# Kernel optimization log

Measured on AMD Instinct MI355X. Metric: run time of the kernel, lower is better.

## Reference

```python
import jax, jax.numpy as jnp
import numpy as np

N_NODES = 15000
N_EDGES = 400000
H_DIM = 128
N_RELS = 237
N_BASES = 100


def rel_graph_conv(x, src, dst, etype, norm, V, comp, loop_w, bias, n_nodes):
    """DGL RelGraphConv with basis regularizer, self_loop=True, bias=True.

    W_r = sum_b comp[r, b] * V[b]; message m_e = (x[src_e] @ W_{etype_e}) * norm_e;
    h[v] = sum_{e: dst_e = v} m_e + x[v] @ loop_w + bias.
    Reordered as sum over bases to avoid materializing per-edge weights:
      h = sum_b segment_sum(coef[etype, b] * norm * x[src], dst) @ V[b]
    """
    x_src = x[src] * norm                      # [E, D] (norm is [E, 1])
    coef = comp[etype]                         # [E, B]
    d_out = V.shape[2]

    def body(acc, cv):
        c, Vb = cv                             # c: [E], Vb: [D, Dout]
        agg = jax.ops.segment_sum(x_src * c[:, None], dst, num_segments=n_nodes)
        return acc + agg @ Vb, None

    init = jnp.zeros((n_nodes, d_out), x.dtype)
    h, _ = jax.lax.scan(body, init, (coef.T, V))  # scan over B bases
    return h + bias + x @ loop_w


def setup_inputs() -> dict:
    key = jax.random.key(0)
    ks = jax.random.split(key, 16)
    s = 1.0 / np.sqrt(H_DIM)
    inp = {
        "nids": jnp.arange(N_NODES, dtype=jnp.int32),
        "src": jax.random.randint(ks[0], (N_EDGES,), 0, N_NODES),
        "dst": jax.random.randint(ks[1], (N_EDGES,), 0, N_NODES),
        "etype": jax.random.randint(ks[2], (N_EDGES,), 0, N_RELS),
        "norm": jax.random.uniform(ks[3], (N_EDGES, 1), dtype=jnp.float32),
        "edge_weights": jax.random.normal(ks[4], (N_EDGES,), dtype=jnp.float32),
        "emb": jax.random.normal(ks[5], (N_NODES, H_DIM), dtype=jnp.float32) * s,
        "V1": jax.random.normal(ks[6], (N_BASES, H_DIM, H_DIM), dtype=jnp.float32) * s,
        "comp1": jax.random.normal(ks[7], (N_RELS, N_BASES), dtype=jnp.float32) * (1.0 / np.sqrt(N_BASES)),
        "loop1": jax.random.normal(ks[8], (H_DIM, H_DIM), dtype=jnp.float32) * s,
        "bias1": jnp.zeros((H_DIM,), dtype=jnp.float32),
        "V2": jax.random.normal(ks[9], (N_BASES, H_DIM, H_DIM), dtype=jnp.float32) * s,
        "comp2": jax.random.normal(ks[10], (N_RELS, N_BASES), dtype=jnp.float32) * (1.0 / np.sqrt(N_BASES)),
        "loop2": jax.random.normal(ks[11], (H_DIM, H_DIM), dtype=jnp.float32) * s,
        "bias2": jnp.zeros((H_DIM,), dtype=jnp.float32),
    }
    return inp


def reference(nids, src, dst, etype, norm, edge_weights, emb, V1, comp1, loop1, bias1, V2, comp2, loop2, bias2):
    # edge_weights is accepted but unused by the original forward.
    x = emb[nids]                                              # embedding lookup
    n = x.shape[0]
    h = jax.nn.relu(rel_graph_conv(x, src, dst, etype, norm, V1, comp1, loop1, bias1, n))
    # dropout(p=0.2) treated as identity (eval mode)
    h = rel_graph_conv(h, src, dst, etype, norm, V2, comp2, loop2, bias2, n)
    return h
```

## Files before the change

kernel.cpp:

```cpp
#include <hip/hip_runtime.h>
#include <hip/hip_bf16.h>


typedef unsigned short u16;
typedef unsigned int   u32;
typedef __bf16 bf16x8 __attribute__((ext_vector_type(8)));
typedef float  f32x4  __attribute__((ext_vector_type(4)));
typedef u32    u32x2  __attribute__((ext_vector_type(2)));

#define N_NODES 15000
#define N_EDGES 400000
#define N_RELS  237
#define N_BASES 100
#define NT_MAX  1800
#define NB_SORT 196
#define CHUNK   2048

__device__ __forceinline__ u32 packbf(float a, float b) {
    u16 lo = __builtin_bit_cast(u16, (__bf16)a);
    u16 hi = __builtin_bit_cast(u16, (__bf16)b);
    return (u32)lo | ((u32)hi << 16);
}
__device__ __forceinline__ u16 bf16bits(float a) {
    return __builtin_bit_cast(u16, (__bf16)a);
}
__device__ __forceinline__ float bfbits2f(u32 hi16) {
    u32 x = hi16 << 16;
    return __builtin_bit_cast(float, x);
}

__global__ __launch_bounds__(256) void histA_kernel(const int* __restrict__ etype,
                                                    int* __restrict__ blockHist) {
    __shared__ int hh[256];
    int tid = threadIdx.x, b = blockIdx.x;
    hh[tid] = 0;
    __syncthreads();
    int e0 = b * CHUNK;
    int e1 = e0 + CHUNK; if (e1 > N_EDGES) e1 = N_EDGES;
    for (int e = e0 + tid; e < e1; e += 256)
        atomicAdd(&hh[etype[e]], 1);
    __syncthreads();
    if (tid < N_RELS) blockHist[tid * NB_SORT + b] = hh[tid];
}

__global__ __launch_bounds__(256) void scanB_kernel(const int* __restrict__ blockHist,
                                                    int* __restrict__ baseOff,
                                                    int2* __restrict__ tiles,
                                                    int* __restrict__ tileCount) {
    __shared__ int h[256], o[256], to[256];
    int tid = threadIdx.x;
    int sum = 0;
    if (tid < N_RELS)
        for (int b = 0; b < NB_SORT; ++b) sum += blockHist[tid * NB_SORT + b];
    h[tid] = (tid < N_RELS) ? sum : 0;
    __syncthreads();
    if (tid == 0) {
        int run = 0, tc = 0;
        for (int r = 0; r < N_RELS; ++r) {
            o[r] = run; run += h[r];
            to[r] = tc; tc += (h[r] + 255) >> 8;
        }
        *tileCount = tc;
    }
    __syncthreads();
    if (tid < N_RELS) {
        int n = h[tid], t0 = to[tid], base = o[tid];
        for (int t = 0; t * 256 < n; ++t) {
            int nE = n - t * 256; if (nE > 256) nE = 256;
            tiles[t0 + t] = make_int2(base + t * 256, (tid << 9) | nE);
        }
        int run = base;
        for (int b = 0; b < NB_SORT; ++b) {
            baseOff[tid * NB_SORT + b] = run;
            run += blockHist[tid * NB_SORT + b];
        }
    }
}

__global__ __launch_bounds__(256) void scatterC_kernel(const int* __restrict__ etype,
                                                       const int* __restrict__ src,
                                                       const float* __restrict__ norm,
                                                       const int* __restrict__ baseOff,
                                                       int* __restrict__ perm,
                                                       int* __restrict__ srcPerm,
                                                       float* __restrict__ normPerm) {
    __shared__ int lcur[256];
    int tid = threadIdx.x, b = blockIdx.x;
    if (tid < N_RELS) lcur[tid] = baseOff[tid * NB_SORT + b];
    __syncthreads();
    int e0 = b * CHUNK;
    int e1 = e0 + CHUNK; if (e1 > N_EDGES) e1 = N_EDGES;
    for (int e = e0 + tid; e < e1; e += 256) {
        int r = etype[e];
        int pos = atomicAdd(&lcur[r], 1);
        perm[pos] = e;
        srcPerm[pos] = src[e];
        normPerm[pos] = norm[e];
    }
}

__global__ __launch_bounds__(256) void zeroDeg_kernel(int* __restrict__ deg) {
    int i = blockIdx.x * 256 + threadIdx.x;
    if (i < N_NODES) deg[i] = 0;
}
__global__ __launch_bounds__(256) void degcnt_kernel(const int* __restrict__ dst,
                                                     int* __restrict__ deg) {
    for (int e = blockIdx.x * 256 + threadIdx.x; e < N_EDGES; e += gridDim.x * 256)
        atomicAdd(&deg[dst[e]], 1);
}
__global__ __launch_bounds__(256) void scanDeg_kernel(const int* __restrict__ deg,
                                                      int* __restrict__ rowptr,
                                                      int* __restrict__ cursor) {
    __shared__ int part[256];
    int tid = threadIdx.x;
    const int R = 59;
    int lo = tid * R, hi = lo + R; if (hi > N_NODES + 1) hi = N_NODES + 1;
    int s = 0;
    for (int i = lo; i < hi; ++i) s += (i < N_NODES) ? deg[i] : 0;
    part[tid] = s;
    __syncthreads();
    if (tid == 0) {
        int run = 0;
        for (int t = 0; t < 256; ++t) { int tmp = part[t]; part[t] = run; run += tmp; }
    }
    __syncthreads();
    int run = part[tid];
    for (int i = lo; i < hi; ++i) {
        rowptr[i] = run; cursor[i] = run;
        run += (i < N_NODES) ? deg[i] : 0;
    }
}
__global__ __launch_bounds__(256) void scatterDst_kernel(const int* __restrict__ dst,
                                                         const int* __restrict__ perm,
                                                         int* __restrict__ cursor,
                                                         int* __restrict__ dstSlots) {
    for (int s = blockIdx.x * 256 + threadIdx.x; s < N_EDGES; s += gridDim.x * 256) {
        int e = perm[s];
        int v = dst[e];
        int pos = atomicAdd(&cursor[v], 1);
        dstSlots[pos] = s;
    }
}

__global__ __launch_bounds__(256) void compcast_kernel(const float* __restrict__ comp,
                                                       u16* __restrict__ compbf) {
    int idx = blockIdx.x * 256 + threadIdx.x;
    if (idx >= 256 * 128) return;
    int r = idx >> 7, b = idx & 127;
    float v = (r < N_RELS && b < N_BASES) ? comp[(size_t)r * N_BASES + b] : 0.f;
    compbf[idx] = bf16bits(v);
}

__global__ __launch_bounds__(256) void vt_kernel(const float* __restrict__ V,
                                                 u16* __restrict__ aimg) {
    __shared__ u16 t[128 * 130];
    int k = blockIdx.x, tid = threadIdx.x;
    #pragma unroll
    for (int i = 0; i < 64; ++i) {
        int idx = i * 256 + tid;
        int b = idx >> 7, col = idx & 127;
        float v = (b < N_BASES) ? V[(size_t)b * 16384 + k * 128 + col] : 0.f;
        t[col * 130 + b] = bf16bits(v);
    }
    __syncthreads();
    #pragma unroll
    for (int i = 0; i < 64; ++i) {
        int idx = i * 256 + tid;
        int col = idx >> 7, b = idx & 127;
        aimg[((size_t)col * 128 + k) * 128 + b] = t[col * 130 + b];
    }
}

__global__ __launch_bounds__(256) void wgemmT_kernel(const u16* __restrict__ compbf,
                                                     const u16* __restrict__ aimg,
                                                     u16* __restrict__ Wbt) {
    __shared__ u16 clds[8192];
    int m0 = blockIdx.x * 64, n0 = blockIdx.y * 128;
    int tid = threadIdx.x, lane = tid & 63, w = tid >> 6;

    bf16x8 afr[2][4];
    #pragma unroll
    for (int n2 = 0; n2 < 2; ++n2) {
        int j = n0 + w * 32 + n2 * 16 + (lane & 15);
        #pragma unroll
        for (int ks = 0; ks < 4; ++ks) {
            int b0 = ks * 32 + (lane >> 4) * 8;
            afr[n2][ks] = *(const bf16x8*)(aimg + (size_t)j * 128 + b0);
        }
    }
    {
        int s = tid >> 2, p = tid & 3;
        const uint4* cr = (const uint4*)(compbf + (size_t)(m0 + s) * 128);
        #pragma unroll
        for (int c = 0; c < 4; ++c) {
            int ch = p * 4 + c;
            *(uint4*)((char*)clds + s * 256 + ((ch * 16) ^ ((s & 7) << 4))) = cr[ch];
        }
    }
    __syncthreads();

    #pragma unroll
    for (int rt = 0; rt < 4; ++rt) {
        bf16x8 cf[4];
        int arow = rt * 16 + (lane & 15);
        #pragma unroll
        for (int ks = 0; ks < 4; ++ks) {
            int k0 = ks * 32 + (lane >> 4) * 8;
            cf[ks] = *(const bf16x8*)((const char*)clds + arow * 256 + ((k0 * 2) ^ ((arow & 7) << 4)));
        }
        f32x4 acc[2];
        acc[0] = (f32x4){0.f, 0.f, 0.f, 0.f};
        acc[1] = (f32x4){0.f, 0.f, 0.f, 0.f};
        #pragma unroll
        for (int ks = 0; ks < 4; ++ks) {
            acc[0] = __builtin_amdgcn_mfma_f32_16x16x32_bf16(afr[0][ks], cf[ks], acc[0], 0, 0, 0);
            acc[1] = __builtin_amdgcn_mfma_f32_16x16x32_bf16(afr[1][ks], cf[ks], acc[1], 0, 0, 0);
        }
        int r = m0 + rt * 16 + (lane & 15);
        if (r < N_RELS) {
            #pragma unroll
            for (int n2 = 0; n2 < 2; ++n2) {
                int jb = n0 + w * 32 + n2 * 16 + ((lane >> 4) << 2);
                u32x2 pk;
                pk.x = packbf(acc[n2][0], acc[n2][1]);
                pk.y = packbf(acc[n2][2], acc[n2][3]);
                *(u32x2*)(Wbt + (size_t)r * 16384 + jb) = pk;
            }
        }
    }
}

__global__ __launch_bounds__(256) void loopT_kernel(const float* __restrict__ lw,
                                                    u16* __restrict__ outT) {
    int tid = threadIdx.x;
    u32* outu = (u32*)outT;
    #pragma unroll
    for (int i = 0; i < 32; ++i) {
        int idx = i * 256 + tid;
        int col = idx >> 6, kk2 = idx & 63;
        float a = lw[(size_t)(2 * kk2) * 128 + col];
        float b = lw[(size_t)(2 * kk2 + 1) * 128 + col];
        outu[col * 64 + kk2] = packbf(a, b);
    }
}

__global__ __launch_bounds__(256) void xbf_kernel(const float* __restrict__ x,
                                                  u16* __restrict__ xbf,
                                                  int reluIn) {
    int i = blockIdx.x * 256 + threadIdx.x;
    if (i >= N_NODES * 16) return;
    const float4* xp = (const float4*)x;
    float4 f0 = xp[i * 2], f1 = xp[i * 2 + 1];
    if (reluIn) {
        f0.x = fmaxf(f0.x, 0.f); f0.y = fmaxf(f0.y, 0.f);
        f0.z = fmaxf(f0.z, 0.f); f0.w = fmaxf(f0.w, 0.f);
        f1.x = fmaxf(f1.x, 0.f); f1.y = fmaxf(f1.y, 0.f);
        f1.z = fmaxf(f1.z, 0.f); f1.w = fmaxf(f1.w, 0.f);
    }
    uint4 pk;
    pk.x = packbf(f0.x, f0.y); pk.y = packbf(f0.z, f0.w);
    pk.z = packbf(f1.x, f1.y); pk.w = packbf(f1.z, f1.w);
    ((uint4*)xbf)[i] = pk;
}

__global__ __launch_bounds__(256) void init_mfma_kernel(const float* __restrict__ xin,
                                                        const u16* __restrict__ lwT,
                                                        const float* __restrict__ bias,
                                                        float* __restrict__ hout,
                                                        int reluIn) {
    __shared__ u16 xlds[8192];
    int v0 = blockIdx.x * 64;
    int tid = threadIdx.x, lane = tid & 63, w = tid >> 6;

    bf16x8 bfr[2][4];
    #pragma unroll
    for (int n2 = 0; n2 < 2; ++n2) {
        int col = w * 32 + n2 * 16 + (lane & 15);
        #pragma unroll
        for (int ks = 0; ks < 4; ++ks) {
            int k0 = ks * 32 + (lane >> 4) * 8;
            bfr[n2][ks] = *(const bf16x8*)(lwT + (size_t)col * 128 + k0);
        }
    }

    {
        int s = tid >> 2, p = tid & 3;
        int row = v0 + s;
        if (row < N_NODES) {
            const float4* xr = (const float4*)(xin + (size_t)row * 128 + p * 32);
            #pragma unroll
            for (int c = 0; c < 4; ++c) {
                float4 f0 = xr[c * 2], f1 = xr[c * 2 + 1];
                if (reluIn) {
                    f0.x = fmaxf(f0.x, 0.f); f0.y = fmaxf(f0.y, 0.f);
                    f0.z = fmaxf(f0.z, 0.f); f0.w = fmaxf(f0.w, 0.f);
                    f1.x = fmaxf(f1.x, 0.f); f1.y = fmaxf(f1.y, 0.f);
                    f1.z = fmaxf(f1.z, 0.f); f1.w = fmaxf(f1.w, 0.f);
                }
                bf16x8 pk;
                pk[0] = (__bf16)f0.x; pk[1] = (__bf16)f0.y;
                pk[2] = (__bf16)f0.z; pk[3] = (__bf16)f0.w;
                pk[4] = (__bf16)f1.x; pk[5] = (__bf16)f1.y;
                pk[6] = (__bf16)f1.z; pk[7] = (__bf16)f1.w;
                int ch = p * 4 + c;
                *(bf16x8*)((char*)xlds + s * 256 + ((ch * 16) ^ ((s & 7) << 4))) = pk;
            }
        } else {
            bf16x8 z = {(__bf16)0.f, (__bf16)0.f, (__bf16)0.f, (__bf16)0.f,
                        (__bf16)0.f, (__bf16)0.f, (__bf16)0.f, (__bf16)0.f};
            #pragma unroll
            for (int c = 0; c < 4; ++c) {
                int ch = p * 4 + c;
                *(bf16x8*)((char*)xlds + s * 256 + ((ch * 16) ^ ((s & 7) << 4))) = z;
            }
        }
    }
    __syncthreads();

    #pragma unroll
    for (int rt = 0; rt < 4; ++rt) {
        bf16x8 af[4];
        int arow = rt * 16 + (lane & 15);
        #pragma unroll
        for (int ks = 0; ks < 4; ++ks) {
            int k0 = ks * 32 + (lane >> 4) * 8;
            af[ks] = *(const bf16x8*)((const char*)xlds + arow * 256 + ((k0 * 2) ^ ((arow & 7) << 4)));
        }
        f32x4 acc[2];
        acc[0] = (f32x4){0.f, 0.f, 0.f, 0.f};
        acc[1] = (f32x4){0.f, 0.f, 0.f, 0.f};
        #pragma unroll
        for (int ks = 0; ks < 4; ++ks) {
            acc[0] = __builtin_amdgcn_mfma_f32_16x16x32_bf16(bfr[0][ks], af[ks], acc[0], 0, 0, 0);
            acc[1] = __builtin_amdgcn_mfma_f32_16x16x32_bf16(bfr[1][ks], af[ks], acc[1], 0, 0, 0);
        }
        int orow = v0 + rt * 16 + (lane & 15);
        if (orow < N_NODES) {
            #pragma unroll
            for (int n2 = 0; n2 < 2; ++n2) {
                int fbase = w * 32 + n2 * 16 + ((lane >> 4) << 2);
                float4 bv = *(const float4*)(bias + fbase);
                float4 o;
                o.x = acc[n2][0] + bv.x; o.y = acc[n2][1] + bv.y;
                o.z = acc[n2][2] + bv.z; o.w = acc[n2][3] + bv.w;
                *(float4*)(hout + (size_t)orow * 128 + fbase) = o;
            }
        }
    }
}

__global__ __launch_bounds__(256) void msg_kernel(const u16* __restrict__ xbf,
                                                  const int* __restrict__ srcPerm,
                                                  const int2* __restrict__ tiles,
                                                  const int* __restrict__ tileCount,
                                                  const u16* __restrict__ WbtT,
                                                  u16* __restrict__ msg) {
    __shared__ u16 xlds[8192];
    int bid = blockIdx.x;
    int tile = (bid & 7) * (NT_MAX / 8) + (bid >> 3);
    if (tile >= *tileCount) return;
    int2 td = tiles[tile];
    int slot0 = td.x;
    int r  = td.y >> 9;
    int nE = td.y & 511;
    int tid = threadIdx.x, lane = tid & 63, w = tid >> 6;

    bf16x8 bfr[2][4];
    #pragma unroll
    for (int n2 = 0; n2 < 2; ++n2) {
        int col = w * 32 + n2 * 16 + (lane & 15);
        #pragma unroll
        for (int ks = 0; ks < 4; ++ks) {
            int k0 = ks * 32 + (lane >> 4) * 8;
            bfr[n2][ks] = *(const bf16x8*)(WbtT + (size_t)r * 16384 + col * 128 + k0);
        }
    }

    for (int s0 = 0; s0 < nE; s0 += 64) {
        int cnt = nE - s0; if (cnt > 64) cnt = 64;
        __syncthreads();
        {
            int s = tid >> 2, p = tid & 3;
            if (s < cnt) {
                int xrow = srcPerm[slot0 + s0 + s];
                const uint4* xr = (const uint4*)(xbf + (size_t)xrow * 128);
                #pragma unroll
                for (int c = 0; c < 4; ++c) {
                    int ch = p * 4 + c;
                    *(uint4*)((char*)xlds + s * 256 + ((ch * 16) ^ ((s & 7) << 4))) = xr[ch];
                }
            } else {
                uint4 z = {0u, 0u, 0u, 0u};
                #pragma unroll
                for (int c = 0; c < 4; ++c) {
                    int ch = p * 4 + c;
                    *(uint4*)((char*)xlds + s * 256 + ((ch * 16) ^ ((s & 7) << 4))) = z;
                }
            }
        }
        __syncthreads();

        #pragma unroll
        for (int rt = 0; rt < 4; ++rt) {
            bf16x8 af[4];
            int arow = rt * 16 + (lane & 15);
            #pragma unroll
            for (int ks = 0; ks < 4; ++ks) {
                int k0 = ks * 32 + (lane >> 4) * 8;
                af[ks] = *(const bf16x8*)((const char*)xlds + arow * 256 + ((k0 * 2) ^ ((arow & 7) << 4)));
            }
            f32x4 acc[2];
            acc[0] = (f32x4){0.f, 0.f, 0.f, 0.f};
            acc[1] = (f32x4){0.f, 0.f, 0.f, 0.f};
            #pragma unroll
            for (int ks = 0; ks < 4; ++ks) {
                acc[0] = __builtin_amdgcn_mfma_f32_16x16x32_bf16(bfr[0][ks], af[ks], acc[0], 0, 0, 0);
                acc[1] = __builtin_amdgcn_mfma_f32_16x16x32_bf16(bfr[1][ks], af[ks], acc[1], 0, 0, 0);
            }
            int srow = rt * 16 + (lane & 15);
            if (srow < cnt) {
                int slot = slot0 + s0 + srow;
                #pragma unroll
                for (int n2 = 0; n2 < 2; ++n2) {
                    int fbase = w * 32 + n2 * 16 + ((lane >> 4) << 2);
                    u32x2 pk;
                    pk.x = packbf(acc[n2][0], acc[n2][1]);
                    pk.y = packbf(acc[n2][2], acc[n2][3]);
                    *(u32x2*)(msg + (size_t)slot * 128 + fbase) = pk;
                }
            }
        }
    }
}

__global__ __launch_bounds__(256) void reduce_kernel(const u32* __restrict__ msg32,
                                                     const float* __restrict__ normPerm,
                                                     const int* __restrict__ rowptr,
                                                     const int* __restrict__ dstSlots,
                                                     float* __restrict__ h) {
    int v = blockIdx.x * 4 + (threadIdx.x >> 6);
    int lane = threadIdx.x & 63;
    if (v >= N_NODES) return;
    int p0 = rowptr[v], p1 = rowptr[v + 1];
    float a0 = 0.f, a1 = 0.f, b0 = 0.f, b1 = 0.f;
    int j = p0;
    for (; j + 3 < p1; j += 4) {
        int s0 = dstSlots[j], s1 = dstSlots[j + 1];
        int s2 = dstSlots[j + 2], s3 = dstSlots[j + 3];
        float n0 = normPerm[s0], n1 = normPerm[s1];
        float n2 = normPerm[s2], n3 = normPerm[s3];
        u32 m0 = __builtin_nontemporal_load(msg32 + (size_t)s0 * 64 + lane);
        u32 m1 = __builtin_nontemporal_load(msg32 + (size_t)s1 * 64 + lane);
        u32 m2 = __builtin_nontemporal_load(msg32 + (size_t)s2 * 64 + lane);
        u32 m3 = __builtin_nontemporal_load(msg32 + (size_t)s3 * 64 + lane);
        a0 += n0 * bfbits2f(m0 & 0xffffu); a1 += n0 * bfbits2f(m0 >> 16);
        b0 += n1 * bfbits2f(m1 & 0xffffu); b1 += n1 * bfbits2f(m1 >> 16);
        a0 += n2 * bfbits2f(m2 & 0xffffu); a1 += n2 * bfbits2f(m2 >> 16);
        b0 += n3 * bfbits2f(m3 & 0xffffu); b1 += n3 * bfbits2f(m3 >> 16);
    }
    for (; j < p1; ++j) {
        int s0 = dstSlots[j];
        float n0 = normPerm[s0];
        u32 m0 = __builtin_nontemporal_load(msg32 + (size_t)s0 * 64 + lane);
        a0 += n0 * bfbits2f(m0 & 0xffffu); a1 += n0 * bfbits2f(m0 >> 16);
    }
    float2 hv = *(float2*)(h + (size_t)v * 128 + lane * 2);
    hv.x += a0 + b0;
    hv.y += a1 + b1;
    *(float2*)(h + (size_t)v * 128 + lane * 2) = hv;
}

__global__ __launch_bounds__(256) void edge_atomic_kernel(const float* __restrict__ x,
                                                          const int* __restrict__ src,
                                                          const int* __restrict__ dst,
                                                          const float* __restrict__ norm,
                                                          const int* __restrict__ perm,
                                                          const int2* __restrict__ tiles,
                                                          const int* __restrict__ tileCount,
                                                          const u16* __restrict__ WbtT,
                                                          float* __restrict__ hout,
                                                          int reluIn) {
    __shared__ u16 xlds[8192];
    __shared__ int dlds[64];
    int bid = blockIdx.x;
    if (bid >= *tileCount) return;
    int2 td = tiles[bid];
    int slot0 = td.x;
    int r  = td.y >> 9;
    int nE = td.y & 511;
    int tid = threadIdx.x, lane = tid & 63, w = tid >> 6;

    bf16x8 bfr[2][4];
    #pragma unroll
    for (int n2 = 0; n2 < 2; ++n2) {
        int col = w * 32 + n2 * 16 + (lane & 15);
        #pragma unroll
        for (int ks = 0; ks < 4; ++ks) {
            int k0 = ks * 32 + (lane >> 4) * 8;
            bfr[n2][ks] = *(const bf16x8*)(WbtT + (size_t)r * 16384 + col * 128 + k0);
        }
    }

    for (int s0 = 0; s0 < nE; s0 += 64) {
        int cnt = nE - s0; if (cnt > 64) cnt = 64;
        __syncthreads();
        {
            int s = tid >> 2, p = tid & 3;
            if (s < cnt) {
                int e = perm[slot0 + s0 + s];
                int xrow = src[e];
                float nm = norm[e];
                if (p == 0) dlds[s] = dst[e];
                const float4* xr = (const float4*)(x + (size_t)xrow * 128 + p * 32);
                #pragma unroll
                for (int c = 0; c < 4; ++c) {
                    float4 f0 = xr[c * 2], f1 = xr[c * 2 + 1];
                    if (reluIn) {
                        f0.x = fmaxf(f0.x, 0.f); f0.y = fmaxf(f0.y, 0.f);
                        f0.z = fmaxf(f0.z, 0.f); f0.w = fmaxf(f0.w, 0.f);
                        f1.x = fmaxf(f1.x, 0.f); f1.y = fmaxf(f1.y, 0.f);
                        f1.z = fmaxf(f1.z, 0.f); f1.w = fmaxf(f1.w, 0.f);
                    }
                    bf16x8 pk;
                    pk[0] = (__bf16)(f0.x * nm); pk[1] = (__bf16)(f0.y * nm);
                    pk[2] = (__bf16)(f0.z * nm); pk[3] = (__bf16)(f0.w * nm);
                    pk[4] = (__bf16)(f1.x * nm); pk[5] = (__bf16)(f1.y * nm);
                    pk[6] = (__bf16)(f1.z * nm); pk[7] = (__bf16)(f1.w * nm);
                    int ch = p * 4 + c;
                    *(bf16x8*)((char*)xlds + s * 256 + ((ch * 16) ^ ((s & 7) << 4))) = pk;
                }
            } else {
                bf16x8 z = {(__bf16)0.f, (__bf16)0.f, (__bf16)0.f, (__bf16)0.f,
                            (__bf16)0.f, (__bf16)0.f, (__bf16)0.f, (__bf16)0.f};
                #pragma unroll
                for (int c = 0; c < 4; ++c) {
                    int ch = p * 4 + c;
                    *(bf16x8*)((char*)xlds + s * 256 + ((ch * 16) ^ ((s & 7) << 4))) = z;
                }
            }
        }
        __syncthreads();

        #pragma unroll
        for (int rt = 0; rt < 4; ++rt) {
            bf16x8 af[4];
            int arow = rt * 16 + (lane & 15);
            #pragma unroll
            for (int ks = 0; ks < 4; ++ks) {
                int k0 = ks * 32 + (lane >> 4) * 8;
                af[ks] = *(const bf16x8*)((const char*)xlds + arow * 256 + ((k0 * 2) ^ ((arow & 7) << 4)));
            }
            f32x4 acc[2];
            acc[0] = (f32x4){0.f, 0.f, 0.f, 0.f};
            acc[1] = (f32x4){0.f, 0.f, 0.f, 0.f};
            #pragma unroll
            for (int ks = 0; ks < 4; ++ks) {
                acc[0] = __builtin_amdgcn_mfma_f32_16x16x32_bf16(bfr[0][ks], af[ks], acc[0], 0, 0, 0);
                acc[1] = __builtin_amdgcn_mfma_f32_16x16x32_bf16(bfr[1][ks], af[ks], acc[1], 0, 0, 0);
            }
            int srow = rt * 16 + (lane & 15);
            if (srow < cnt) {
                int d = dlds[srow];
                #pragma unroll
                for (int n2 = 0; n2 < 2; ++n2) {
                    float* hp = hout + (size_t)d * 128 + w * 32 + n2 * 16 + ((lane >> 4) << 2);
                    #pragma unroll
                    for (int reg = 0; reg < 4; ++reg) atomicAdd(hp + reg, acc[n2][reg]);
                }
            }
        }
    }
}

extern "C" void kernel_launch(void* const* d_in, const int* in_sizes, int n_in,
                              void* d_out, int out_size, void* d_ws, size_t ws_size,
                              hipStream_t stream) {
    const int*   src   = (const int*)  d_in[1];
    const int*   dst   = (const int*)  d_in[2];
    const int*   etype = (const int*)  d_in[3];
    const float* norm  = (const float*)d_in[4];
    const float* emb   = (const float*)d_in[6];
    const float* V1    = (const float*)d_in[7];
    const float* comp1 = (const float*)d_in[8];
    const float* loop1 = (const float*)d_in[9];
    const float* bias1 = (const float*)d_in[10];
    const float* V2    = (const float*)d_in[11];
    const float* comp2 = (const float*)d_in[12];
    const float* loop2 = (const float*)d_in[13];
    const float* bias2 = (const float*)d_in[14];
    float* out = (float*)d_out;

    char* ws = (char*)d_ws;
    size_t off = 0;
    auto carve = [&](size_t bytes) -> void* {
        void* p = ws + off;
        off += (bytes + 255) & ~(size_t)255;
        return p;
    };
    const size_t WB = (size_t)N_RELS * 16384 * 2;
    u16* Wbt1      = (u16*)carve(WB);
    u16* Wbt2      = (u16*)carve(WB);
    float* h1      = (float*)carve((size_t)N_NODES * 128 * 4);
    int*  perm     = (int*)carve((size_t)N_EDGES * 4);
    int*  srcPerm  = (int*)carve((size_t)N_EDGES * 4);
    float* normPerm= (float*)carve((size_t)N_EDGES * 4);
    int*  blockHist= (int*)carve((size_t)N_RELS * NB_SORT * 4);
    int*  baseOff  = (int*)carve((size_t)N_RELS * NB_SORT * 4);
    int2* tiles    = (int2*)carve((size_t)NT_MAX * 8);
    int*  tileCnt  = (int*)carve(256);
    u16*  lwT1     = (u16*)carve(128 * 128 * 2);
    u16*  lwT2     = (u16*)carve(128 * 128 * 2);
    u16*  compbf1  = (u16*)carve(256 * 128 * 2);
    u16*  compbf2  = (u16*)carve(256 * 128 * 2);
    u16*  aimg     = (u16*)carve((size_t)16384 * 128 * 2);
    int*  deg      = (int*)carve((size_t)N_NODES * 4);
    int*  rowptr   = (int*)carve((size_t)(N_NODES + 1) * 4);
    int*  cursor   = (int*)carve((size_t)(N_NODES + 1) * 4);
    int*  dstSlots = (int*)carve((size_t)N_EDGES * 4);
    u16*  xbf      = (u16*)carve((size_t)N_NODES * 128 * 2);
    u16*  msg      = (u16*)carve((size_t)N_EDGES * 128 * 2);
    bool twoPhase = (off <= ws_size);

    histA_kernel<<<NB_SORT, 256, 0, stream>>>(etype, blockHist);
    scanB_kernel<<<1, 256, 0, stream>>>(blockHist, baseOff, tiles, tileCnt);
    scatterC_kernel<<<NB_SORT, 256, 0, stream>>>(etype, src, norm, baseOff,
                                                 perm, srcPerm, normPerm);

    if (twoPhase) {
        zeroDeg_kernel<<<59, 256, 0, stream>>>(deg);
        degcnt_kernel<<<391, 256, 0, stream>>>(dst, deg);
        scanDeg_kernel<<<1, 256, 0, stream>>>(deg, rowptr, cursor);
        scatterDst_kernel<<<391, 256, 0, stream>>>(dst, perm, cursor, dstSlots);
    }

    dim3 wgg(4, 128);
    compcast_kernel<<<128, 256, 0, stream>>>(comp1, compbf1);
    compcast_kernel<<<128, 256, 0, stream>>>(comp2, compbf2);
    vt_kernel<<<128, 256, 0, stream>>>(V1, aimg);
    wgemmT_kernel<<<wgg, 256, 0, stream>>>(compbf1, aimg, Wbt1);
    vt_kernel<<<128, 256, 0, stream>>>(V2, aimg);
    wgemmT_kernel<<<wgg, 256, 0, stream>>>(compbf2, aimg, Wbt2);
    loopT_kernel<<<1, 256, 0, stream>>>(loop1, lwT1);
    loopT_kernel<<<1, 256, 0, stream>>>(loop2, lwT2);

    if (twoPhase) {
        xbf_kernel<<<938, 256, 0, stream>>>(emb, xbf, 0);
        init_mfma_kernel<<<235, 256, 0, stream>>>(emb, lwT1, bias1, h1, 0);
        msg_kernel<<<NT_MAX, 256, 0, stream>>>(xbf, srcPerm, tiles, tileCnt,
                                               Wbt1, msg);
        reduce_kernel<<<3750, 256, 0, stream>>>((const u32*)msg, normPerm,
                                                rowptr, dstSlots, h1);
        xbf_kernel<<<938, 256, 0, stream>>>(h1, xbf, 1);
        init_mfma_kernel<<<235, 256, 0, stream>>>(h1, lwT2, bias2, out, 1);
        msg_kernel<<<NT_MAX, 256, 0, stream>>>(xbf, srcPerm, tiles, tileCnt,
                                               Wbt2, msg);
        reduce_kernel<<<3750, 256, 0, stream>>>((const u32*)msg, normPerm,
                                                rowptr, dstSlots, out);
    } else {
        init_mfma_kernel<<<235, 256, 0, stream>>>(emb, lwT1, bias1, h1, 0);
        edge_atomic_kernel<<<NT_MAX, 256, 0, stream>>>(emb, src, dst, norm, perm, tiles,
                                                       tileCnt, Wbt1, h1, 0);
        init_mfma_kernel<<<235, 256, 0, stream>>>(h1, lwT2, bias2, out, 1);
        edge_atomic_kernel<<<NT_MAX, 256, 0, stream>>>(h1, src, dst, norm, perm, tiles,
                                                       tileCnt, Wbt2, out, 1);
    }
}
```

Baseline: 413.5 us.

## Double-buffer msg gather, fuse relu+bf16 cast into reduce, parallelize loopT

The message kernel now prefetches the next 64-row chunk of source features into registers while the current chunk runs its MFMAs, writing into an alternate LDS buffer. This hides gather latency behind compute at the cost of doubled LDS and more registers. The first-layer reduce kernel also writes the relu'd bf16 copy of h1 directly, removing a separate xbf conversion pass. The loop-weight transpose is spread across 32 blocks instead of one.

```diff
diff --git a/kernel.cpp b/kernel.cpp
--- a/kernel.cpp
+++ b/kernel.cpp
@@ -232,16 +232,12 @@
 
 __global__ __launch_bounds__(256) void loopT_kernel(const float* __restrict__ lw,
                                                     u16* __restrict__ outT) {
-    int tid = threadIdx.x;
-    u32* outu = (u32*)outT;
-    #pragma unroll
-    for (int i = 0; i < 32; ++i) {
-        int idx = i * 256 + tid;
-        int col = idx >> 6, kk2 = idx & 63;
-        float a = lw[(size_t)(2 * kk2) * 128 + col];
-        float b = lw[(size_t)(2 * kk2 + 1) * 128 + col];
-        outu[col * 64 + kk2] = packbf(a, b);
-    }
+    int idx = blockIdx.x * 256 + threadIdx.x;
+    if (idx >= 8192) return;
+    int col = idx >> 6, kk2 = idx & 63;
+    float a = lw[(size_t)(2 * kk2) * 128 + col];
+    float b = lw[(size_t)(2 * kk2 + 1) * 128 + col];
+    ((u32*)outT)[col * 64 + kk2] = packbf(a, b);
 }
 
 __global__ __launch_bounds__(256) void xbf_kernel(const float* __restrict__ x,
@@ -355,7 +351,7 @@
                                                   const int* __restrict__ tileCount,
                                                   const u16* __restrict__ WbtT,
                                                   u16* __restrict__ msg) {
-    __shared__ u16 xlds[8192];
+    __shared__ u16 xlds[2][8192];
     int bid = blockIdx.x;
     int tile = (bid & 7) * (NT_MAX / 8) + (bid >> 3);
     if (tile >= *tileCount) return;
@@ -364,6 +360,7 @@
     int r  = td.y >> 9;
     int nE = td.y & 511;
     int tid = threadIdx.x, lane = tid & 63, w = tid >> 6;
+    int gs = tid >> 2, gp = tid & 3;
 
     bf16x8 bfr[2][4];
     #pragma unroll
@@ -376,30 +373,39 @@
         }
     }
 
+    uint4 g[4];
+    auto gather = [&](int s0) {
+        int cnt = nE - s0; if (cnt > 64) cnt = 64;
+        if (gs < cnt) {
+            int xrow = srcPerm[slot0 + s0 + gs];
+            const uint4* xr = (const uint4*)(xbf + (size_t)xrow * 128);
+            #pragma unroll
+            for (int c = 0; c < 4; ++c) g[c] = xr[gp * 4 + c];
+        } else {
+            uint4 z = {0u, 0u, 0u, 0u};
+            #pragma unroll
+            for (int c = 0; c < 4; ++c) g[c] = z;
+        }
+    };
+    auto writeLds = [&](u16* buf) {
+        #pragma unroll
+        for (int c = 0; c < 4; ++c) {
+            int ch = gp * 4 + c;
+            *(uint4*)((char*)buf + gs * 256 + ((ch * 16) ^ ((gs & 7) << 4))) = g[c];
+        }
+    };
+
+    gather(0);
+    writeLds(xlds[0]);
+    __syncthreads();
+    int cur = 0;
+
     for (int s0 = 0; s0 < nE; s0 += 64) {
         int cnt = nE - s0; if (cnt > 64) cnt = 64;
-        __syncthreads();
-        {
-            int s = tid >> 2, p = tid & 3;
-            if (s < cnt) {
-                int xrow = srcPerm[slot0 + s0 + s];
-                const uint4* xr = (const uint4*)(xbf + (size_t)xrow * 128);
-                #pragma unroll
-                for (int c = 0; c < 4; ++c) {
-                    int ch = p * 4 + c;
-                    *(uint4*)((char*)xlds + s * 256 + ((ch * 16) ^ ((s & 7) << 4))) = xr[ch];
-                }
-            } else {
-                uint4 z = {0u, 0u, 0u, 0u};
-                #pragma unroll
-                for (int c = 0; c < 4; ++c) {
-                    int ch = p * 4 + c;
-                    *(uint4*)((char*)xlds + s * 256 + ((ch * 16) ^ ((s & 7) << 4))) = z;
-                }
-            }
-        }
-        __syncthreads();
-
+        int nxt = s0 + 64;
+        if (nxt < nE) gather(nxt);
+
+        const u16* buf = xlds[cur];
         #pragma unroll
         for (int rt = 0; rt < 4; ++rt) {
             bf16x8 af[4];
@@ -407,7 +413,7 @@
             #pragma unroll
             for (int ks = 0; ks < 4; ++ks) {
                 int k0 = ks * 32 + (lane >> 4) * 8;
-                af[ks] = *(const bf16x8*)((const char*)xlds + arow * 256 + ((k0 * 2) ^ ((arow & 7) << 4)));
+                af[ks] = *(const bf16x8*)((const char*)buf + arow * 256 + ((k0 * 2) ^ ((arow & 7) << 4)));
             }
             f32x4 acc[2];
             acc[0] = (f32x4){0.f, 0.f, 0.f, 0.f};
@@ -430,6 +436,12 @@
                 }
             }
         }
+
+        if (nxt >= nE) break;
+        __syncthreads();
+        writeLds(xlds[cur ^ 1]);
+        __syncthreads();
+        cur ^= 1;
     }
 }
 
@@ -437,7 +449,8 @@
                                                      const float* __restrict__ normPerm,
                                                      const int* __restrict__ rowptr,
                                                      const int* __restrict__ dstSlots,
-                                                     float* __restrict__ h) {
+                                                     float* __restrict__ h,
+                                                     u32* __restrict__ xbfOut) {
     int v = blockIdx.x * 4 + (threadIdx.x >> 6);
     int lane = threadIdx.x & 63;
     if (v >= N_NODES) return;
@@ -468,6 +481,10 @@
     hv.x += a0 + b0;
     hv.y += a1 + b1;
     *(float2*)(h + (size_t)v * 128 + lane * 2) = hv;
+    if (xbfOut) {
+        float rx = fmaxf(hv.x, 0.f), ry = fmaxf(hv.y, 0.f);
+        xbfOut[(size_t)v * 64 + lane] = packbf(rx, ry);
+    }
 }
 
 __global__ __launch_bounds__(256) void edge_atomic_kernel(const float* __restrict__ x,
@@ -640,8 +657,8 @@
     wgemmT_kernel<<<wgg, 256, 0, stream>>>(compbf1, aimg, Wbt1);
     vt_kernel<<<128, 256, 0, stream>>>(V2, aimg);
     wgemmT_kernel<<<wgg, 256, 0, stream>>>(compbf2, aimg, Wbt2);
-    loopT_kernel<<<1, 256, 0, stream>>>(loop1, lwT1);
-    loopT_kernel<<<1, 256, 0, stream>>>(loop2, lwT2);
+    loopT_kernel<<<32, 256, 0, stream>>>(loop1, lwT1);
+    loopT_kernel<<<32, 256, 0, stream>>>(loop2, lwT2);
 
     if (twoPhase) {
         xbf_kernel<<<938, 256, 0, stream>>>(emb, xbf, 0);
@@ -649,13 +666,12 @@
         msg_kernel<<<NT_MAX, 256, 0, stream>>>(xbf, srcPerm, tiles, tileCnt,
                                                Wbt1, msg);
         reduce_kernel<<<3750, 256, 0, stream>>>((const u32*)msg, normPerm,
-                                                rowptr, dstSlots, h1);
-        xbf_kernel<<<938, 256, 0, stream>>>(h1, xbf, 1);
+                                                rowptr, dstSlots, h1, (u32*)xbf);
         init_mfma_kernel<<<235, 256, 0, stream>>>(h1, lwT2, bias2, out, 1);
         msg_kernel<<<NT_MAX, 256, 0, stream>>>(xbf, srcPerm, tiles, tileCnt,
                                                Wbt2, msg);
         reduce_kernel<<<3750, 256, 0, stream>>>((const u32*)msg, normPerm,
-                                                rowptr, dstSlots, out);
+                                                rowptr, dstSlots, out, (u32*)0);
     } else {
         init_mfma_kernel<<<235, 256, 0, stream>>>(emb, lwT1, bias1, h1, 0);
         edge_atomic_kernel<<<NT_MAX, 256, 0, stream>>>(emb, src, dst, norm, perm, tiles,
```

Result: faster. 397.7 us (-3.8%).
